# Kernel optimization log

Measured on AMD Instinct MI355X. Metric: run time of the kernel, lower is better.

## Reference

```python
import jax, jax.numpy as jnp
import numpy as np

NUM_LAYERS = 3
HIDDEN = 64
NUM_CLASSES = 4096
LN_EPS = 1e-5


def setup_inputs() -> dict:
    key = jax.random.key(0)
    ks = jax.random.split(key, 8)
    B, N, E, H = 8, NUM_CLASSES, 131072, HIDDEN
    node_features = jax.random.normal(ks[0], (B, N, H), dtype=jnp.float32)
    edge_indices = jax.random.randint(ks[1], (B, 2, E), 0, N, dtype=jnp.int64)
    edge_attrs = jax.random.normal(ks[2], (B, E, H), dtype=jnp.float32)
    # GraphConvolutionLayer params (xavier_uniform weight, zero bias) per layer
    limit = np.sqrt(6.0 / (H + H)).astype(np.float32)
    W = jax.random.uniform(ks[3], (NUM_LAYERS, H, H), minval=-limit, maxval=limit, dtype=jnp.float32)
    b = jnp.zeros((NUM_LAYERS, H), dtype=jnp.float32)
    gamma = jnp.ones((NUM_LAYERS, H), dtype=jnp.float32)
    beta = jnp.zeros((NUM_LAYERS, H), dtype=jnp.float32)
    global_emb = 0.02 * jax.random.normal(ks[4], (N, H), dtype=jnp.float32)
    return {
        "node_features": node_features,
        "edge_indices": edge_indices,
        "edge_attrs": edge_attrs,
        "W": W,
        "b": b,
        "gamma": gamma,
        "beta": beta,
        "global_emb": global_emb,
    }


def _layer_norm(x, g, bt):
    mu = jnp.mean(x, axis=-1, keepdims=True)
    var = jnp.mean((x - mu) ** 2, axis=-1, keepdims=True)
    return (x - mu) * jax.lax.rsqrt(var + LN_EPS) * g + bt


def reference(node_features, edge_indices, edge_attrs, W, b, gamma, beta, global_emb):
    N = node_features.shape[1]

    def per_graph(x0, ei, ea):
        # presence mask computed on raw node features [N, 1]
        presence = (jnp.sum(x0, axis=1) != 0).astype(x0.dtype)[:, None]
        src, dst = ei[0], ei[1]
        x = x0
        for i in range(NUM_LAYERS):
            residual = x
            h = x @ W[i]                                   # [N, H]
            msg = h[src] * ea                              # gather + edge gate [E, H]
            out = jax.ops.segment_sum(msg, dst, num_segments=N) + b[i]
            out = jax.nn.relu(out)
            out = _layer_norm(out, gamma[i], beta[i])
            x = out + residual if i > 0 else out
        return x * presence + global_emb * (1.0 - presence)

    return jax.vmap(per_graph)(node_features, edge_indices, edge_attrs)
```

## Files before the change

kernel.cpp:

```cpp
#include <hip/hip_runtime.h>

#define GB 8
#define GN 4096
#define GH 64
#define GE 131072
#define LN_EPS 1e-5f
#define NBIN (GB * GN)
#define TOTE (GB * GE)

static __device__ __forceinline__ float bfu(unsigned short u) {
    union { float f; unsigned int i; } v; v.i = ((unsigned int)u) << 16; return v.f;
}
static __device__ __forceinline__ unsigned short f2bf(float f) {
    union { float f; unsigned int u; } v; v.f = f;
    unsigned int u = v.u;
    return (unsigned short)((u + 0x7FFFu + ((u >> 16) & 1u)) >> 16);
}

__global__ void k_init(const float* __restrict__ nf, float* __restrict__ pres) {
    int w = (blockIdx.x * blockDim.x + threadIdx.x) >> 6;
    int lane = threadIdx.x & 63;
    if (w >= NBIN) return;
    float v = nf[(size_t)w * GH + lane];
    #pragma unroll
    for (int o = 1; o < 64; o <<= 1) v += __shfl_xor(v, o, 64);
    if (lane == 0) pres[w] = (v != 0.0f) ? 1.0f : 0.0f;
}

__global__ void k_hist(const int* __restrict__ ei, int* __restrict__ hist) {
    int t = blockIdx.x * blockDim.x + threadIdx.x;
    int b = t >> 17, e = t & (GE - 1);
    int dst = ei[(b << 18) + GE + e];
    atomicAdd(&hist[(b << 12) + dst], 1);
}

__global__ void k_scan(const int* __restrict__ hist, int* __restrict__ off,
                       int* __restrict__ cur) {
    __shared__ int part[256];
    int b = blockIdx.x;
    int t = threadIdx.x;
    int base = (b << 12) + t * 16;
    int c[16];
    int s = 0;
    #pragma unroll
    for (int i = 0; i < 16; ++i) { c[i] = hist[base + i]; s += c[i]; }
    part[t] = s;
    __syncthreads();
    for (int o = 1; o < 256; o <<= 1) {
        int u = (t >= o) ? part[t - o] : 0;
        __syncthreads();
        part[t] += u;
        __syncthreads();
    }
    int p = b * GE + part[t] - s;
    #pragma unroll
    for (int i = 0; i < 16; ++i) { off[base + i] = p; cur[base + i] = p; p += c[i]; }
    if (b == GB - 1 && t == 255) off[NBIN] = TOTE;
}

__global__ void k_fillperm(const int* __restrict__ ei, int* __restrict__ cur,
                           const float* __restrict__ ea,
                           int* __restrict__ sSrc, unsigned short* __restrict__ ea_s) {
    int grp = (blockIdx.x * blockDim.x + threadIdx.x) >> 4;
    if (grp >= TOTE) return;
    int sub  = threadIdx.x & 15;
    int lane = threadIdx.x & 63;
    int b = grp >> 17, e = grp & (GE - 1);
    int dst = ei[(b << 18) + GE + e];
    int pos = 0;
    if (sub == 0) pos = atomicAdd(&cur[(b << 12) + dst], 1);
    pos = __shfl(pos, lane & ~15, 64);
    float4 v = *reinterpret_cast<const float4*>(ea + ((size_t)grp << 6) + (sub << 2));
    ushort4 o;
    o.x = f2bf(v.x); o.y = f2bf(v.y); o.z = f2bf(v.z); o.w = f2bf(v.w);
    *reinterpret_cast<ushort4*>(ea_s + ((size_t)pos << 6) + (sub << 2)) = o;
    if (sub == 0) sSrc[pos] = ei[(b << 18) + e];
}

__global__ void k_gemm(const float* __restrict__ x, const float* __restrict__ W,
                       unsigned short* __restrict__ h, int layer) {
    __shared__ float Wl[GH * GH];
    for (int i = threadIdx.x; i < GH * GH; i += blockDim.x)
        Wl[i] = W[layer * GH * GH + i];
    __syncthreads();
    int w = (blockIdx.x * blockDim.x + threadIdx.x) >> 6;
    int lane = threadIdx.x & 63;
    if (w >= NBIN) return;
    float xv = x[(size_t)w * GH + lane];
    float acc = 0.0f;
    #pragma unroll
    for (int k = 0; k < GH; ++k)
        acc = fmaf(__shfl(xv, k, 64), Wl[k * GH + lane], acc);
    h[(size_t)w * GH + lane] = f2bf(acc);
}

__global__ void k_gather(const int* __restrict__ off, const int* __restrict__ sSrc,
                         const unsigned short* __restrict__ ea_s,
                         const unsigned short* __restrict__ h,
                         const float* __restrict__ bias, const float* __restrict__ gam,
                         const float* __restrict__ bet,
                         float* __restrict__ x, const float* __restrict__ pres,
                         const float* __restrict__ ge, float* __restrict__ out,
                         int layer) {
    int w = (blockIdx.x * blockDim.x + threadIdx.x) >> 6;
    int lane = threadIdx.x & 63;
    if (w >= NBIN) return;
    int b = w >> 12;
    int beg = off[w], end = off[w + 1];
    int cnt = end - beg;
    const unsigned short* hb = h + (((size_t)b) << 12) * GH;
    int fg = (lane & 15) << 2;
    int g  = lane >> 4;

    float4 acc = make_float4(0.f, 0.f, 0.f, 0.f);
    for (int base = 0; base < cnt; base += 64) {
        int n = min(cnt - base, 64);
        int sv = (lane < n) ? sSrc[beg + base + lane] : 0;
        for (int j = 0; j < n; j += 8) {
            int j0 = j + g, j1 = j + 4 + g;
            int s0 = __shfl(sv, j0);
            int s1 = __shfl(sv, j1);
            if (j0 < n) {
                ushort4 ev = *reinterpret_cast<const ushort4*>(ea_s + ((size_t)(beg + base + j0) << 6) + fg);
                ushort4 hv = *reinterpret_cast<const ushort4*>(hb + ((size_t)s0 << 6) + fg);
                acc.x = fmaf(bfu(ev.x), bfu(hv.x), acc.x);
                acc.y = fmaf(bfu(ev.y), bfu(hv.y), acc.y);
                acc.z = fmaf(bfu(ev.z), bfu(hv.z), acc.z);
                acc.w = fmaf(bfu(ev.w), bfu(hv.w), acc.w);
            }
            if (j1 < n) {
                ushort4 ev = *reinterpret_cast<const ushort4*>(ea_s + ((size_t)(beg + base + j1) << 6) + fg);
                ushort4 hv = *reinterpret_cast<const ushort4*>(hb + ((size_t)s1 << 6) + fg);
                acc.x = fmaf(bfu(ev.x), bfu(hv.x), acc.x);
                acc.y = fmaf(bfu(ev.y), bfu(hv.y), acc.y);
                acc.z = fmaf(bfu(ev.z), bfu(hv.z), acc.z);
                acc.w = fmaf(bfu(ev.w), bfu(hv.w), acc.w);
            }
        }
    }
    #pragma unroll
    for (int o = 16; o < 64; o <<= 1) {
        acc.x += __shfl_xor(acc.x, o, 64);
        acc.y += __shfl_xor(acc.y, o, 64);
        acc.z += __shfl_xor(acc.z, o, 64);
        acc.w += __shfl_xor(acc.w, o, 64);
    }
    int srcl = lane >> 2;
    float c0 = __shfl(acc.x, srcl);
    float c1 = __shfl(acc.y, srcl);
    float c2 = __shfl(acc.z, srcl);
    float c3 = __shfl(acc.w, srcl);
    int cc = lane & 3;
    float v = (cc == 0) ? c0 : (cc == 1) ? c1 : (cc == 2) ? c2 : c3;

    v = fmaxf(v + bias[layer * GH + lane], 0.0f);
    float s = v;
    #pragma unroll
    for (int o = 1; o < 64; o <<= 1) s += __shfl_xor(s, o, 64);
    float mu = s * (1.0f / GH);
    float d = v - mu;
    float q = d * d;
    #pragma unroll
    for (int o = 1; o < 64; o <<= 1) q += __shfl_xor(q, o, 64);
    float var = q * (1.0f / GH);
    float y = d * rsqrtf(var + LN_EPS) * gam[layer * GH + lane] + bet[layer * GH + lane];
    size_t idx = (size_t)w * GH + lane;
    if (layer > 0) y += x[idx];
    if (layer < 2) {
        x[idx] = y;
    } else {
        float p = pres[w];
        float g2 = ge[(size_t)(w & (GN - 1)) * GH + lane];
        out[idx] = y * p + g2 * (1.0f - p);
    }
}

extern "C" void kernel_launch(void* const* d_in, const int* in_sizes, int n_in,
                              void* d_out, int out_size, void* d_ws, size_t ws_size,
                              hipStream_t stream) {
    const float* nf = (const float*)d_in[0];
    const int* ei   = (const int*)d_in[1];
    const float* ea = (const float*)d_in[2];
    const float* W  = (const float*)d_in[3];
    const float* bb = (const float*)d_in[4];
    const float* gg = (const float*)d_in[5];
    const float* be = (const float*)d_in[6];
    const float* ge = (const float*)d_in[7];
    float* out = (float*)d_out;

    float* x    = (float*)d_ws;
    float* pres = x + (size_t)NBIN * GH;
    int* off    = (int*)(pres + NBIN);
    int* cur    = off + NBIN + 1;
    int* hist   = cur + NBIN;
    int* sSrc   = hist + NBIN;
    unsigned short* h_s  = (unsigned short*)(sSrc + TOTE);
    unsigned short* ea_s = h_s + (size_t)NBIN * GH;

    hipMemsetAsync(hist, 0, NBIN * sizeof(int), stream);
    k_init<<<NBIN / 4, 256, 0, stream>>>(nf, pres);
    k_hist<<<TOTE / 256, 256, 0, stream>>>(ei, hist);
    k_scan<<<GB, 256, 0, stream>>>(hist, off, cur);
    k_fillperm<<<TOTE / 16, 256, 0, stream>>>(ei, cur, ea, sSrc, ea_s);

    for (int l = 0; l < 3; ++l) {
        k_gemm<<<NBIN / 4, 256, 0, stream>>>(l == 0 ? nf : x, W, h_s, l);
        k_gather<<<NBIN / 4, 256, 0, stream>>>(off, sSrc, ea_s, h_s, bb, gg, be,
                                               x, pres, ge, out, l);
    }
}
```

Baseline: 426.8 us.

## Remap gather kernel to 8 lanes per node with 16-byte loads

```diff
diff --git a/kernel.cpp b/kernel.cpp
--- a/kernel.cpp
+++ b/kernel.cpp
@@ -8,13 +8,26 @@
 #define NBIN (GB * GN)
 #define TOTE (GB * GE)
 
-static __device__ __forceinline__ float bfu(unsigned short u) {
-    union { float f; unsigned int i; } v; v.i = ((unsigned int)u) << 16; return v.f;
-}
 static __device__ __forceinline__ unsigned short f2bf(float f) {
     union { float f; unsigned int u; } v; v.f = f;
     unsigned int u = v.u;
     return (unsigned short)((u + 0x7FFFu + ((u >> 16) & 1u)) >> 16);
+}
+static __device__ __forceinline__ void bf2x(unsigned int u, float& lo, float& hi) {
+    union { float f; unsigned int i; } a, b;
+    a.i = u << 16; b.i = u & 0xFFFF0000u;
+    lo = a.f; hi = b.f;
+}
+static __device__ __forceinline__ void fma8(uint4 ev, uint4 hv, float4& a0, float4& a1) {
+    float el, eh, hl, hh;
+    bf2x(ev.x, el, eh); bf2x(hv.x, hl, hh);
+    a0.x = fmaf(el, hl, a0.x); a0.y = fmaf(eh, hh, a0.y);
+    bf2x(ev.y, el, eh); bf2x(hv.y, hl, hh);
+    a0.z = fmaf(el, hl, a0.z); a0.w = fmaf(eh, hh, a0.w);
+    bf2x(ev.z, el, eh); bf2x(hv.z, hl, hh);
+    a1.x = fmaf(el, hl, a1.x); a1.y = fmaf(eh, hh, a1.y);
+    bf2x(ev.w, el, eh); bf2x(hv.w, hl, hh);
+    a1.z = fmaf(el, hl, a1.z); a1.w = fmaf(eh, hh, a1.w);
 }
 
 __global__ void k_init(const float* __restrict__ nf, float* __restrict__ pres) {
@@ -102,76 +115,89 @@
                          float* __restrict__ x, const float* __restrict__ pres,
                          const float* __restrict__ ge, float* __restrict__ out,
                          int layer) {
-    int w = (blockIdx.x * blockDim.x + threadIdx.x) >> 6;
-    int lane = threadIdx.x & 63;
+    int w = (blockIdx.x * blockDim.x + threadIdx.x) >> 3;
     if (w >= NBIN) return;
+    int sub = threadIdx.x & 7;
     int b = w >> 12;
     int beg = off[w], end = off[w + 1];
-    int cnt = end - beg;
-    const unsigned short* hb = h + (((size_t)b) << 12) * GH;
-    int fg = (lane & 15) << 2;
-    int g  = lane >> 4;
-
-    float4 acc = make_float4(0.f, 0.f, 0.f, 0.f);
-    for (int base = 0; base < cnt; base += 64) {
-        int n = min(cnt - base, 64);
-        int sv = (lane < n) ? sSrc[beg + base + lane] : 0;
-        for (int j = 0; j < n; j += 8) {
-            int j0 = j + g, j1 = j + 4 + g;
-            int s0 = __shfl(sv, j0);
-            int s1 = __shfl(sv, j1);
-            if (j0 < n) {
-                ushort4 ev = *reinterpret_cast<const ushort4*>(ea_s + ((size_t)(beg + base + j0) << 6) + fg);
-                ushort4 hv = *reinterpret_cast<const ushort4*>(hb + ((size_t)s0 << 6) + fg);
-                acc.x = fmaf(bfu(ev.x), bfu(hv.x), acc.x);
-                acc.y = fmaf(bfu(ev.y), bfu(hv.y), acc.y);
-                acc.z = fmaf(bfu(ev.z), bfu(hv.z), acc.z);
-                acc.w = fmaf(bfu(ev.w), bfu(hv.w), acc.w);
-            }
-            if (j1 < n) {
-                ushort4 ev = *reinterpret_cast<const ushort4*>(ea_s + ((size_t)(beg + base + j1) << 6) + fg);
-                ushort4 hv = *reinterpret_cast<const ushort4*>(hb + ((size_t)s1 << 6) + fg);
-                acc.x = fmaf(bfu(ev.x), bfu(hv.x), acc.x);
-                acc.y = fmaf(bfu(ev.y), bfu(hv.y), acc.y);
-                acc.z = fmaf(bfu(ev.z), bfu(hv.z), acc.z);
-                acc.w = fmaf(bfu(ev.w), bfu(hv.w), acc.w);
-            }
-        }
-    }
-    #pragma unroll
-    for (int o = 16; o < 64; o <<= 1) {
-        acc.x += __shfl_xor(acc.x, o, 64);
-        acc.y += __shfl_xor(acc.y, o, 64);
-        acc.z += __shfl_xor(acc.z, o, 64);
-        acc.w += __shfl_xor(acc.w, o, 64);
-    }
-    int srcl = lane >> 2;
-    float c0 = __shfl(acc.x, srcl);
-    float c1 = __shfl(acc.y, srcl);
-    float c2 = __shfl(acc.z, srcl);
-    float c3 = __shfl(acc.w, srcl);
-    int cc = lane & 3;
-    float v = (cc == 0) ? c0 : (cc == 1) ? c1 : (cc == 2) ? c2 : c3;
-
-    v = fmaxf(v + bias[layer * GH + lane], 0.0f);
-    float s = v;
-    #pragma unroll
-    for (int o = 1; o < 64; o <<= 1) s += __shfl_xor(s, o, 64);
+    const unsigned short* hb = h + ((((size_t)b) << 12) * GH);
+
+    float4 a0 = make_float4(0.f, 0.f, 0.f, 0.f);
+    float4 a1 = make_float4(0.f, 0.f, 0.f, 0.f);
+    int e = beg;
+    for (; e + 4 <= end; e += 4) {
+        int s0 = sSrc[e + 0];
+        int s1 = sSrc[e + 1];
+        int s2 = sSrc[e + 2];
+        int s3 = sSrc[e + 3];
+        uint4 ev0 = *reinterpret_cast<const uint4*>(ea_s + (((size_t)(e + 0)) << 6) + (sub << 3));
+        uint4 ev1 = *reinterpret_cast<const uint4*>(ea_s + (((size_t)(e + 1)) << 6) + (sub << 3));
+        uint4 ev2 = *reinterpret_cast<const uint4*>(ea_s + (((size_t)(e + 2)) << 6) + (sub << 3));
+        uint4 ev3 = *reinterpret_cast<const uint4*>(ea_s + (((size_t)(e + 3)) << 6) + (sub << 3));
+        uint4 hv0 = *reinterpret_cast<const uint4*>(hb + (((size_t)s0) << 6) + (sub << 3));
+        uint4 hv1 = *reinterpret_cast<const uint4*>(hb + (((size_t)s1) << 6) + (sub << 3));
+        uint4 hv2 = *reinterpret_cast<const uint4*>(hb + (((size_t)s2) << 6) + (sub << 3));
+        uint4 hv3 = *reinterpret_cast<const uint4*>(hb + (((size_t)s3) << 6) + (sub << 3));
+        fma8(ev0, hv0, a0, a1);
+        fma8(ev1, hv1, a0, a1);
+        fma8(ev2, hv2, a0, a1);
+        fma8(ev3, hv3, a0, a1);
+    }
+    for (; e < end; ++e) {
+        int s0 = sSrc[e];
+        uint4 ev = *reinterpret_cast<const uint4*>(ea_s + (((size_t)e) << 6) + (sub << 3));
+        uint4 hv = *reinterpret_cast<const uint4*>(hb + (((size_t)s0) << 6) + (sub << 3));
+        fma8(ev, hv, a0, a1);
+    }
+
+    const float4* bias4 = reinterpret_cast<const float4*>(bias + layer * GH + (sub << 3));
+    float4 b0 = bias4[0], b1 = bias4[1];
+    float4 v0, v1;
+    v0.x = fmaxf(a0.x + b0.x, 0.f); v0.y = fmaxf(a0.y + b0.y, 0.f);
+    v0.z = fmaxf(a0.z + b0.z, 0.f); v0.w = fmaxf(a0.w + b0.w, 0.f);
+    v1.x = fmaxf(a1.x + b1.x, 0.f); v1.y = fmaxf(a1.y + b1.y, 0.f);
+    v1.z = fmaxf(a1.z + b1.z, 0.f); v1.w = fmaxf(a1.w + b1.w, 0.f);
+    float s = v0.x + v0.y + v0.z + v0.w + v1.x + v1.y + v1.z + v1.w;
+    #pragma unroll
+    for (int o = 1; o < 8; o <<= 1) s += __shfl_xor(s, o, 64);
     float mu = s * (1.0f / GH);
-    float d = v - mu;
-    float q = d * d;
-    #pragma unroll
-    for (int o = 1; o < 64; o <<= 1) q += __shfl_xor(q, o, 64);
-    float var = q * (1.0f / GH);
-    float y = d * rsqrtf(var + LN_EPS) * gam[layer * GH + lane] + bet[layer * GH + lane];
-    size_t idx = (size_t)w * GH + lane;
-    if (layer > 0) y += x[idx];
+    float4 d0, d1;
+    d0.x = v0.x - mu; d0.y = v0.y - mu; d0.z = v0.z - mu; d0.w = v0.w - mu;
+    d1.x = v1.x - mu; d1.y = v1.y - mu; d1.z = v1.z - mu; d1.w = v1.w - mu;
+    float q = d0.x*d0.x + d0.y*d0.y + d0.z*d0.z + d0.w*d0.w
+            + d1.x*d1.x + d1.y*d1.y + d1.z*d1.z + d1.w*d1.w;
+    #pragma unroll
+    for (int o = 1; o < 8; o <<= 1) q += __shfl_xor(q, o, 64);
+    float r = rsqrtf(q * (1.0f / GH) + LN_EPS);
+    const float4* gam4 = reinterpret_cast<const float4*>(gam + layer * GH + (sub << 3));
+    const float4* bet4 = reinterpret_cast<const float4*>(bet + layer * GH + (sub << 3));
+    float4 g0 = gam4[0], g1 = gam4[1];
+    float4 t0 = bet4[0], t1 = bet4[1];
+    float4 y0, y1;
+    y0.x = d0.x * r * g0.x + t0.x; y0.y = d0.y * r * g0.y + t0.y;
+    y0.z = d0.z * r * g0.z + t0.z; y0.w = d0.w * r * g0.w + t0.w;
+    y1.x = d1.x * r * g1.x + t1.x; y1.y = d1.y * r * g1.y + t1.y;
+    y1.z = d1.z * r * g1.z + t1.z; y1.w = d1.w * r * g1.w + t1.w;
+
+    float4* xp = reinterpret_cast<float4*>(x + (size_t)w * GH + (sub << 3));
+    if (layer > 0) {
+        float4 x0 = xp[0], x1 = xp[1];
+        y0.x += x0.x; y0.y += x0.y; y0.z += x0.z; y0.w += x0.w;
+        y1.x += x1.x; y1.y += x1.y; y1.z += x1.z; y1.w += x1.w;
+    }
     if (layer < 2) {
-        x[idx] = y;
+        xp[0] = y0; xp[1] = y1;
     } else {
         float p = pres[w];
-        float g2 = ge[(size_t)(w & (GN - 1)) * GH + lane];
-        out[idx] = y * p + g2 * (1.0f - p);
+        const float4* ge4 = reinterpret_cast<const float4*>(ge + (size_t)(w & (GN - 1)) * GH + (sub << 3));
+        float4 e0 = ge4[0], e1 = ge4[1];
+        float4 o0, o1;
+        o0.x = y0.x * p + e0.x * (1.f - p); o0.y = y0.y * p + e0.y * (1.f - p);
+        o0.z = y0.z * p + e0.z * (1.f - p); o0.w = y0.w * p + e0.w * (1.f - p);
+        o1.x = y1.x * p + e1.x * (1.f - p); o1.y = y1.y * p + e1.y * (1.f - p);
+        o1.z = y1.z * p + e1.z * (1.f - p); o1.w = y1.w * p + e1.w * (1.f - p);
+        float4* op = reinterpret_cast<float4*>(out + (size_t)w * GH + (sub << 3));
+        op[0] = o0; op[1] = o1;
     }
 }
 
@@ -205,7 +231,7 @@
 
     for (int l = 0; l < 3; ++l) {
         k_gemm<<<NBIN / 4, 256, 0, stream>>>(l == 0 ? nf : x, W, h_s, l);
-        k_gather<<<NBIN / 4, 256, 0, stream>>>(off, sSrc, ea_s, h_s, bb, gg, be,
-                                               x, pres, ge, out, l);
-    }
-}
+        k_gather<<<NBIN * 8 / 256, 256, 0, stream>>>(off, sSrc, ea_s, h_s, bb, gg, be,
+                                                     x, pres, ge, out, l);
+    }
+}
```

New measurement: 428.1 us. About the same (+0.3%).
